# Kernel optimization log

Hardware: AMD Instinct MI355X
Metric: run time of the kernel (lower is better)

The kernel has to match this reference:

```python
import jax, jax.numpy as jnp
import numpy as np

N = 100000   # nodes
E = 1600000  # edges
G = 64       # graphs in batch
F_IN = 128
H = 128
SV = 64
AD = 32


def setup_inputs() -> dict:
    key = jax.random.key(0)
    ks = jax.random.split(key, 12)
    s = 0.05
    return {
        "x": jax.random.normal(ks[0], (N, F_IN), jnp.float32),
        "edge_index": jax.random.randint(ks[1], (2, E), 0, N, dtype=jnp.int64),
        "batch": jnp.sort(jax.random.randint(ks[2], (N,), 0, G, dtype=jnp.int64)),
        "state_vector": jax.random.normal(ks[3], (G, SV), jnp.float32),
        "action": jax.random.normal(ks[4], (G, AD), jnp.float32),
        "W1": jax.random.normal(ks[5], (F_IN, H), jnp.float32) * s,
        "b1": jnp.zeros((H,), jnp.float32),
        "W2": jax.random.normal(ks[6], (H, H), jnp.float32) * s,
        "b2": jnp.zeros((H,), jnp.float32),
        "Wf1": jax.random.normal(ks[7], (H + SV + AD, 256), jnp.float32) * s,
        "bf1": jnp.zeros((256,), jnp.float32),
        "Wf2": jax.random.normal(ks[8], (256, 256), jnp.float32) * s,
        "bf2": jnp.zeros((256,), jnp.float32),
        "Wo": jax.random.normal(ks[9], (256, 1), jnp.float32) * s,
        "bo": jnp.zeros((1,), jnp.float32),
    }


def gcn_conv(x, W, b, src, dst, deg_inv_sqrt):
    # PyG GCNConv: h = x @ W; aggregate D^-1/2 (A+I) D^-1/2 h; + b
    h = x @ W
    norm = deg_inv_sqrt[src] * deg_inv_sqrt[dst]          # [E]
    agg = jax.ops.segment_sum(h[src] * norm[:, None], dst, num_segments=N)
    agg = agg + h * (deg_inv_sqrt * deg_inv_sqrt)[:, None]  # self loops
    return agg + b


def reference(x, edge_index, batch, state_vector, action,
              W1, b1, W2, b2, Wf1, bf1, Wf2, bf2, Wo, bo):
    src, dst = edge_index[0], edge_index[1]
    # degree after adding self loops (aggregation index = dst, PyG default flow)
    deg = jax.ops.segment_sum(jnp.ones((E,), jnp.float32), dst, num_segments=N) + 1.0
    deg_inv_sqrt = jax.lax.rsqrt(deg)

    h = jax.nn.relu(gcn_conv(x, W1, b1, src, dst, deg_inv_sqrt))
    h = jax.nn.relu(gcn_conv(h, W2, b2, src, dst, deg_inv_sqrt))

    # global_mean_pool over graph ids
    sums = jax.ops.segment_sum(h, batch, num_segments=G)
    cnts = jax.ops.segment_sum(jnp.ones((N,), jnp.float32), batch, num_segments=G)
    pooled = sums / jnp.maximum(cnts, 1.0)[:, None]       # [G, H]

    z = jnp.concatenate([pooled, state_vector, action], axis=1)  # [G, H+SV+AD]
    z = jax.nn.relu(z @ Wf1 + bf1)
    z = jax.nn.relu(z @ Wf2 + bf2)
    return z @ Wo + bo                                     # [G, 1]
```

## Files before the change

### kernel.cpp

```cpp
#include <hip/hip_runtime.h>
#include <hip/hip_bf16.h>
#include <stdint.h>

#define N_NODES 100000
#define N_EDGES 1600000
#define N_GRAPHS 64
#define HDIM 128

#define BUCKET_SHIFT 9
#define NBUCK ((N_NODES + 511) >> 9)
#define CAP 9216
#define SCAT_CHUNK 4096
#define SCAT_NBLK ((N_EDGES + SCAT_CHUNK - 1) / SCAT_CHUNK)

typedef __bf16 bf16x8 __attribute__((ext_vector_type(8)));
typedef float f32x4 __attribute__((ext_vector_type(4)));
typedef float f32x2 __attribute__((ext_vector_type(2)));

__global__ void init_kernel(int* __restrict__ gcur, float* __restrict__ psum) {
    int i = blockIdx.x * blockDim.x + threadIdx.x;
    if (i < NBUCK) gcur[i] = i * CAP;
    int j = i - NBUCK;
    if (j >= 0 && j < N_GRAPHS * HDIM) psum[j] = 0.f;
}

__global__ __launch_bounds__(256) void transpose_w2_kernel(const float* __restrict__ W1,
                                                           const float* __restrict__ W2,
                                                           __hip_bfloat16* __restrict__ Wt1,
                                                           __hip_bfloat16* __restrict__ Wt2) {
    int bid = blockIdx.x;
    const float* W = (bid < 64) ? W1 : W2;
    __hip_bfloat16* Wt = (bid < 64) ? Wt1 : Wt2;
    int bb = bid & 63;
    int n = bb * 2 + (threadIdx.x >> 7);
    int k = threadIdx.x & 127;
    Wt[n * 128 + k] = __float2bfloat16(W[k * 128 + n]);
}

__global__ __launch_bounds__(256) void scatter_kernel(const int* __restrict__ src,
                                                      const int* __restrict__ dst,
                                                      int* __restrict__ gcur,
                                                      int* __restrict__ sorted, int E) {
    __shared__ int hist[NBUCK];
    __shared__ int base_s[NBUCK];
    int tid = threadIdx.x;
    int e0 = blockIdx.x * SCAT_CHUNK;
    int sv[SCAT_CHUNK / 256], dv[SCAT_CHUNK / 256];
#pragma unroll
    for (int j = 0; j < SCAT_CHUNK / 256; j++) {
        int e = e0 + (j << 8) + tid;
        if (e < E) { sv[j] = src[e]; dv[j] = dst[e]; } else { sv[j] = -1; dv[j] = -1; }
    }
    if (tid < NBUCK) hist[tid] = 0;
    __syncthreads();
#pragma unroll
    for (int j = 0; j < SCAT_CHUNK / 256; j++)
        if (dv[j] >= 0) atomicAdd(&hist[dv[j] >> BUCKET_SHIFT], 1);
    __syncthreads();
    if (tid < NBUCK) {
        int c = hist[tid];
        base_s[tid] = (c > 0) ? atomicAdd(&gcur[tid], c) : 0;
    }
    __syncthreads();
    if (tid < NBUCK) hist[tid] = 0;
    __syncthreads();
#pragma unroll
    for (int j = 0; j < SCAT_CHUNK / 256; j++) {
        if (dv[j] >= 0) {
            int b = dv[j] >> BUCKET_SHIFT;
            int idx = atomicAdd(&hist[b], 1);
            sorted[base_s[b] + idx] = ((dv[j] & 511) << 17) | sv[j];
        }
    }
}

__global__ __launch_bounds__(256) void bucket_build_kernel(const int* __restrict__ sorted,
                                                           const int* __restrict__ gcur,
                                                           int2* __restrict__ rs2,
                                                           float* __restrict__ dis,
                                                           int* __restrict__ csr_src) {
    __shared__ int cnt[512];
    __shared__ int excl[512];
    __shared__ int ps[256];
    int b = blockIdx.x, tid = threadIdx.x;
    cnt[tid] = 0; cnt[tid + 256] = 0;
    __syncthreads();
    int node0 = b << BUCKET_SHIFT;
    int lo = b * CAP, hi = gcur[b];
    for (int i = lo + tid; i < hi; i += 256)
        atomicAdd(&cnt[((unsigned)sorted[i]) >> 17], 1);
    __syncthreads();
    int c0 = cnt[2 * tid], c1 = cnt[2 * tid + 1];
    ps[tid] = c0 + c1;
    __syncthreads();
#pragma unroll
    for (int off = 1; off < 256; off <<= 1) {
        int t = (tid >= off) ? ps[tid - off] : 0;
        __syncthreads();
        ps[tid] += t;
        __syncthreads();
    }
    int pex = ps[tid] - (c0 + c1);
    excl[2 * tid] = pex;
    excl[2 * tid + 1] = pex + c0;
    __syncthreads();
#pragma unroll
    for (int k = 0; k < 2; k++) {
        int li = tid + k * 256;
        int node = node0 + li;
        if (node < N_NODES) {
            int st = lo + excl[li];
            int c = cnt[li];
            rs2[node] = make_int2(st, st + c);
            dis[node] = rsqrtf((float)c + 1.0f);
        }
    }
    cnt[tid] = 0; cnt[tid + 256] = 0;
    __syncthreads();
    for (int i = lo + tid; i < hi; i += 256) {
        int v = sorted[i];
        int li = ((unsigned)v) >> 17;
        int idx = atomicAdd(&cnt[li], 1);
        csr_src[lo + excl[li] + idx] = v & 0x1FFFF;
    }
}

__global__ void graph_bounds_kernel(const int* __restrict__ batch, int* __restrict__ gstart,
                                    int n, int G) {
    int i = blockIdx.x * blockDim.x + threadIdx.x;
    if (i >= n) return;
    int b = batch[i];
    int prev = (i == 0) ? -1 : batch[i - 1];
    for (int g = prev + 1; g <= b; ++g) gstart[g] = i;
    if (i == n - 1) {
        for (int g = b + 1; g <= G; ++g) gstart[g] = n;
    }
}

template<bool A_FP32>
__global__ __launch_bounds__(256) void gemm_mfma_kernel(const void* __restrict__ Av,
                                                        const __hip_bfloat16* __restrict__ Wt,
                                                        const float* __restrict__ scale,
                                                        unsigned char* __restrict__ C, int nrows) {
    __shared__ float Cs[64 * 132];
    int tid = threadIdx.x;
    int wave = tid >> 6, lane = tid & 63;
    int quad = lane >> 4, l16 = lane & 15;
    int row0 = blockIdx.x * 64;
    int arow = row0 + wave * 16 + l16;
    int arow_c = min(arow, nrows - 1);

    const __hip_bfloat16* A16 = (const __hip_bfloat16*)Av;
    const float* A32 = (const float*)Av;

    f32x4 acc[8];
#pragma unroll
    for (int t = 0; t < 8; t++) acc[t] = (f32x4){0.f, 0.f, 0.f, 0.f};

#pragma unroll
    for (int kt = 0; kt < 4; kt++) {
        int kbase = kt * 32 + quad * 8;
        union { bf16x8 v; __hip_bfloat16 h[8]; uint4 u; } au;
        if (A_FP32) {
            const float* ap = A32 + (size_t)arow_c * 128 + kbase;
            float4 u0 = *(const float4*)ap;
            float4 u1 = *(const float4*)(ap + 4);
            au.h[0] = __float2bfloat16(u0.x); au.h[1] = __float2bfloat16(u0.y);
            au.h[2] = __float2bfloat16(u0.z); au.h[3] = __float2bfloat16(u0.w);
            au.h[4] = __float2bfloat16(u1.x); au.h[5] = __float2bfloat16(u1.y);
            au.h[6] = __float2bfloat16(u1.z); au.h[7] = __float2bfloat16(u1.w);
        } else {
            au.u = *(const uint4*)(A16 + (size_t)arow_c * 128 + kbase);
        }
#pragma unroll
        for (int t = 0; t < 8; t++) {
            bf16x8 b = *(const bf16x8*)(Wt + (size_t)(t * 16 + l16) * 128 + kbase);
            acc[t] = __builtin_amdgcn_mfma_f32_16x16x32_bf16(au.v, b, acc[t], 0, 0, 0);
        }
    }

    int rbase = wave * 16 + quad * 4;
    float s[4];
#pragma unroll
    for (int r = 0; r < 4; r++) s[r] = scale[min(row0 + rbase + r, nrows - 1)];
#pragma unroll
    for (int t = 0; t < 8; t++) {
#pragma unroll
        for (int r = 0; r < 4; r++)
            Cs[(rbase + r) * 132 + t * 16 + l16] = acc[t][r] * s[r];
    }
    __syncthreads();

#pragma unroll
    for (int p = 0; p < 4; p++) {
        int g = p * 256 + tid;
        int row = g >> 4, c8 = (g & 15) * 8;
        int grow = row0 + row;
        if (grow < nrows) {
            const float* cp = &Cs[row * 132 + c8];
            float4 v0 = *(const float4*)cp;
            float4 v1 = *(const float4*)(cp + 4);
            int w0 = __builtin_amdgcn_cvt_pk_fp8_f32(v0.x, v0.y, 0, false);
            w0 = __builtin_amdgcn_cvt_pk_fp8_f32(v0.z, v0.w, w0, true);
            int w1 = __builtin_amdgcn_cvt_pk_fp8_f32(v1.x, v1.y, 0, false);
            w1 = __builtin_amdgcn_cvt_pk_fp8_f32(v1.z, v1.w, w1, true);
            *(uint2*)(C + (size_t)grow * 128 + c8) = make_uint2((unsigned)w0, (unsigned)w1);
        }
    }
}

__device__ __forceinline__ void accum8(float* acc, uint2 u) {
    f32x2 d0 = __builtin_amdgcn_cvt_pk_f32_fp8((int)u.x, false);
    f32x2 d1 = __builtin_amdgcn_cvt_pk_f32_fp8((int)u.x, true);
    f32x2 d2 = __builtin_amdgcn_cvt_pk_f32_fp8((int)u.y, false);
    f32x2 d3 = __builtin_amdgcn_cvt_pk_f32_fp8((int)u.y, true);
    acc[0] += d0[0]; acc[1] += d0[1]; acc[2] += d1[0]; acc[3] += d1[1];
    acc[4] += d2[0]; acc[5] += d2[1]; acc[6] += d3[0]; acc[7] += d3[1];
}

__global__ __launch_bounds__(256) void agg_kernel(const unsigned char* __restrict__ h8,
                                                  const float* __restrict__ dis,
                                                  const int2* __restrict__ rs2,
                                                  const int* __restrict__ csr_src,
                                                  const float* __restrict__ bias,
                                                  __hip_bfloat16* __restrict__ out, int n) {
    int node = blockIdx.x * 4 + (threadIdx.x >> 6);
    if (node >= n) return;
    int lane = threadIdx.x & 63;
    int q = lane >> 4, f = lane & 15;
    float acc[8];
#pragma unroll
    for (int j = 0; j < 8; j++) acc[j] = 0.f;
    int2 se = rs2[node];
    int i = se.x, i1 = se.y;
    for (; i + 8 <= i1; i += 8) {
        int s0 = csr_src[i + q];
        int s1 = csr_src[i + 4 + q];
        uint2 u0 = *(const uint2*)(h8 + (size_t)s0 * 128 + f * 8);
        uint2 u1 = *(const uint2*)(h8 + (size_t)s1 * 128 + f * 8);
        accum8(acc, u0);
        accum8(acc, u1);
    }
    for (; i + 4 <= i1; i += 4) {
        int s = csr_src[i + q];
        uint2 u = *(const uint2*)(h8 + (size_t)s * 128 + f * 8);
        accum8(acc, u);
    }
    if (i < i1) {
        bool valid = (i + q) < i1;
        int e = valid ? (i + q) : (i1 - 1);
        int s = csr_src[e];
        uint2 u = *(const uint2*)(h8 + (size_t)s * 128 + f * 8);
        if (valid) accum8(acc, u);
    }
    if (q == 0) {
        uint2 u = *(const uint2*)(h8 + (size_t)node * 128 + f * 8);
        accum8(acc, u);
    }
#pragma unroll
    for (int j = 0; j < 8; j++) {
        float v = acc[j];
        v += __shfl_down(v, 32, 64);
        v += __shfl_down(v, 16, 64);
        acc[j] = v;
    }
    if (q == 0) {
        float dn = dis[node];
        float4 b0 = *(const float4*)(bias + f * 8);
        float4 b1 = *(const float4*)(bias + f * 8 + 4);
        float r0 = fmaxf(fmaf(acc[0], dn, b0.x), 0.f);
        float r1 = fmaxf(fmaf(acc[1], dn, b0.y), 0.f);
        float r2 = fmaxf(fmaf(acc[2], dn, b0.z), 0.f);
        float r3 = fmaxf(fmaf(acc[3], dn, b0.w), 0.f);
        float r4 = fmaxf(fmaf(acc[4], dn, b1.x), 0.f);
        float r5 = fmaxf(fmaf(acc[5], dn, b1.y), 0.f);
        float r6 = fmaxf(fmaf(acc[6], dn, b1.z), 0.f);
        float r7 = fmaxf(fmaf(acc[7], dn, b1.w), 0.f);
        __hip_bfloat162 p0 = __float22bfloat162_rn(make_float2(r0, r1));
        __hip_bfloat162 p1 = __float22bfloat162_rn(make_float2(r2, r3));
        __hip_bfloat162 p2 = __float22bfloat162_rn(make_float2(r4, r5));
        __hip_bfloat162 p3 = __float22bfloat162_rn(make_float2(r6, r7));
        uint4 pk;
        pk.x = *(unsigned int*)&p0; pk.y = *(unsigned int*)&p1;
        pk.z = *(unsigned int*)&p2; pk.w = *(unsigned int*)&p3;
        *(uint4*)(out + (size_t)node * 128 + f * 8) = pk;
    }
}

#define POOL_ROWS 128
__global__ __launch_bounds__(256) void pool_kernel(const __hip_bfloat16* __restrict__ h,
                                                   const int* __restrict__ batch,
                                                   const int* __restrict__ gstart,
                                                   float* __restrict__ psum, int n) {
    __shared__ float red[16 * 128];
    int tid = threadIdx.x;
    int rr = tid >> 4, fg = tid & 15;
    int r0 = blockIdx.x * POOL_ROWS;
    if (r0 >= n) return;
    int r1 = min(n, r0 + POOL_ROWS);
    int g = batch[r0];
    int seg_lo = r0;
    while (seg_lo < r1) {
        while (gstart[g + 1] <= seg_lo) g++;
        int seg_hi = min(r1, gstart[g + 1]);
        float a[8];
#pragma unroll
        for (int j = 0; j < 8; j++) a[j] = 0.f;
        for (int r = seg_lo + rr; r < seg_hi; r += 16) {
            uint4 u = *(const uint4*)(h + (size_t)r * 128 + fg * 8);
            float2 f0 = __bfloat1622float2(*(__hip_bfloat162*)&u.x);
            float2 f1 = __bfloat1622float2(*(__hip_bfloat162*)&u.y);
            float2 f2 = __bfloat1622float2(*(__hip_bfloat162*)&u.z);
            float2 f3 = __bfloat1622float2(*(__hip_bfloat162*)&u.w);
            a[0] += f0.x; a[1] += f0.y; a[2] += f1.x; a[3] += f1.y;
            a[4] += f2.x; a[5] += f2.y; a[6] += f3.x; a[7] += f3.y;
        }
        *(float4*)&red[rr * 128 + fg * 8] = make_float4(a[0], a[1], a[2], a[3]);
        *(float4*)&red[rr * 128 + fg * 8 + 4] = make_float4(a[4], a[5], a[6], a[7]);
        __syncthreads();
        if (tid < 128) {
            float s = 0.f;
#pragma unroll
            for (int k = 0; k < 16; k++) s += red[k * 128 + tid];
            atomicAdd(&psum[g * 128 + tid], s);
        }
        __syncthreads();
        seg_lo = seg_hi;
    }
}

__global__ __launch_bounds__(256) void mlp_kernel(const float* __restrict__ psum,
                                                  const int* __restrict__ gstart,
                                                  const float* __restrict__ sv,
                                                  const float* __restrict__ act,
                                                  const float* __restrict__ Wf1,
                                                  const float* __restrict__ bf1,
                                                  const float* __restrict__ Wf2,
                                                  const float* __restrict__ bf2,
                                                  const float* __restrict__ Wo,
                                                  const float* __restrict__ bo,
                                                  float* __restrict__ out) {
    int g = blockIdx.x, tid = threadIdx.x;
    __shared__ float z[224];
    __shared__ float z1[256];
    __shared__ float red[256];
    if (tid < 128) {
        int c = gstart[g + 1] - gstart[g];
        float cnt = fmaxf((float)c, 1.f);
        z[tid] = psum[g * 128 + tid] / cnt;
    } else if (tid < 192) {
        z[tid] = sv[g * 64 + (tid - 128)];
    } else if (tid < 224) {
        z[tid] = act[g * 32 + (tid - 192)];
    }
    __syncthreads();
    float a = bf1[tid];
    for (int k = 0; k < 224; k++) a = fmaf(z[k], Wf1[k * 256 + tid], a);
    z1[tid] = fmaxf(a, 0.f);
    __syncthreads();
    float b = bf2[tid];
    for (int k = 0; k < 256; k++) b = fmaf(z1[k], Wf2[k * 256 + tid], b);
    b = fmaxf(b, 0.f);
    red[tid] = b * Wo[tid];
    __syncthreads();
    for (int off = 128; off > 0; off >>= 1) {
        if (tid < off) red[tid] += red[tid + off];
        __syncthreads();
    }
    if (tid == 0) out[g] = red[0] + bo[0];
}

extern "C" void kernel_launch(void* const* d_in, const int* in_sizes, int n_in,
                              void* d_out, int out_size, void* d_ws, size_t ws_size,
                              hipStream_t stream) {
    const float* x   = (const float*)d_in[0];
    const int*   eidx = (const int*)d_in[1];
    const int*   batch = (const int*)d_in[2];
    const float* sv  = (const float*)d_in[3];
    const float* act = (const float*)d_in[4];
    const float* W1  = (const float*)d_in[5];
    const float* b1  = (const float*)d_in[6];
    const float* W2  = (const float*)d_in[7];
    const float* b2  = (const float*)d_in[8];
    const float* Wf1 = (const float*)d_in[9];
    const float* bf1 = (const float*)d_in[10];
    const float* Wf2 = (const float*)d_in[11];
    const float* bf2 = (const float*)d_in[12];
    const float* Wo  = (const float*)d_in[13];
    const float* bo  = (const float*)d_in[14];
    float* out = (float*)d_out;

    const int* srcp = eidx;
    const int* dstp = eidx + N_EDGES;

    char* w = (char*)d_ws;
    int* gcur = (int*)w;               w += (size_t)NBUCK * 4;
    float* psum = (float*)w;           w += (size_t)N_GRAPHS * HDIM * 4;
    int2* rs2 = (int2*)w;              w += (size_t)N_NODES * 8;
    float* dis = (float*)w;            w += (size_t)N_NODES * 4;
    int* gstart = (int*)w;             w += (size_t)(N_GRAPHS + 1) * 4;
    w = (char*)(((uintptr_t)w + 255) & ~(uintptr_t)255);
    int* csr_src = (int*)w;            w += (size_t)NBUCK * CAP * 4;
    w = (char*)(((uintptr_t)w + 255) & ~(uintptr_t)255);
    int* sorted = (int*)w;             w += (size_t)NBUCK * CAP * 4;
    w = (char*)(((uintptr_t)w + 255) & ~(uintptr_t)255);
    __hip_bfloat16* Wt1 = (__hip_bfloat16*)w;   w += (size_t)HDIM * HDIM * 2;
    __hip_bfloat16* Wt2 = (__hip_bfloat16*)w;   w += (size_t)HDIM * HDIM * 2;
    w = (char*)(((uintptr_t)w + 255) & ~(uintptr_t)255);
    unsigned char* hbuf = (unsigned char*)w;    w += (size_t)N_NODES * HDIM;
    w = (char*)(((uintptr_t)w + 255) & ~(uintptr_t)255);
    __hip_bfloat16* abuf = (__hip_bfloat16*)w;  w += (size_t)N_NODES * HDIM * 2;

    init_kernel<<<(NBUCK + N_GRAPHS * HDIM + 255) / 256, 256, 0, stream>>>(gcur, psum);
    transpose_w2_kernel<<<128, 256, 0, stream>>>(W1, W2, Wt1, Wt2);

    scatter_kernel<<<SCAT_NBLK, 256, 0, stream>>>(srcp, dstp, gcur, sorted, N_EDGES);
    bucket_build_kernel<<<NBUCK, 256, 0, stream>>>(sorted, gcur, rs2, dis, csr_src);
    graph_bounds_kernel<<<(N_NODES + 255) / 256, 256, 0, stream>>>(batch, gstart, N_NODES, N_GRAPHS);

    int gemm_blocks = (N_NODES + 63) / 64;
    int agg_blocks = (N_NODES + 3) / 4;

    gemm_mfma_kernel<true><<<gemm_blocks, 256, 0, stream>>>(x, Wt1, dis, hbuf, N_NODES);
    agg_kernel<<<agg_blocks, 256, 0, stream>>>(hbuf, dis, rs2, csr_src, b1, abuf, N_NODES);
    gemm_mfma_kernel<false><<<gemm_blocks, 256, 0, stream>>>(abuf, Wt2, dis, hbuf, N_NODES);
    agg_kernel<<<agg_blocks, 256, 0, stream>>>(hbuf, dis, rs2, csr_src, b2, abuf, N_NODES);

    pool_kernel<<<(N_NODES + POOL_ROWS - 1) / POOL_ROWS, 256, 0, stream>>>(abuf, batch, gstart, psum, N_NODES);
    mlp_kernel<<<N_GRAPHS, 256, 0, stream>>>(psum, gstart, sv, act, Wf1, bf1, Wf2, bf2, Wo, bo, out);
}
```

Before: 347.4 us.

## Merge setup kernels, stage bucket edges in LDS, double scatter chunk

Folds init, weight transpose and graph-bounds computation into one setup kernel, which removes two launches. The bucket-build kernel now copies each bucket's edges into shared memory once instead of reading global memory twice. The scatter chunk size is doubled, which halves the block count and per-block histogram overhead but raises register pressure and lowers parallelism. The extra 36KB of LDS per block may reduce occupancy of bucket_build.

```diff
diff --git a/kernel.cpp b/kernel.cpp
--- a/kernel.cpp
+++ b/kernel.cpp
@@ -10,32 +10,48 @@
 #define BUCKET_SHIFT 9
 #define NBUCK ((N_NODES + 511) >> 9)
 #define CAP 9216
-#define SCAT_CHUNK 4096
+#define SCAT_CHUNK 8192
 #define SCAT_NBLK ((N_EDGES + SCAT_CHUNK - 1) / SCAT_CHUNK)
+#define GB_NBLK ((N_NODES + 255) / 256)
 
 typedef __bf16 bf16x8 __attribute__((ext_vector_type(8)));
 typedef float f32x4 __attribute__((ext_vector_type(4)));
 typedef float f32x2 __attribute__((ext_vector_type(2)));
 
-__global__ void init_kernel(int* __restrict__ gcur, float* __restrict__ psum) {
-    int i = blockIdx.x * blockDim.x + threadIdx.x;
-    if (i < NBUCK) gcur[i] = i * CAP;
-    int j = i - NBUCK;
-    if (j >= 0 && j < N_GRAPHS * HDIM) psum[j] = 0.f;
-}
-
-__global__ __launch_bounds__(256) void transpose_w2_kernel(const float* __restrict__ W1,
-                                                           const float* __restrict__ W2,
-                                                           __hip_bfloat16* __restrict__ Wt1,
-                                                           __hip_bfloat16* __restrict__ Wt2) {
+__global__ __launch_bounds__(256) void setup_kernel(const int* __restrict__ batch,
+                                                    int* __restrict__ gstart,
+                                                    const float* __restrict__ W1,
+                                                    const float* __restrict__ W2,
+                                                    __hip_bfloat16* __restrict__ Wt1,
+                                                    __hip_bfloat16* __restrict__ Wt2,
+                                                    int* __restrict__ gcur,
+                                                    float* __restrict__ psum) {
     int bid = blockIdx.x;
-    const float* W = (bid < 64) ? W1 : W2;
-    __hip_bfloat16* Wt = (bid < 64) ? Wt1 : Wt2;
-    int bb = bid & 63;
-    int n = bb * 2 + (threadIdx.x >> 7);
-    int k = threadIdx.x & 127;
-    Wt[n * 128 + k] = __float2bfloat16(W[k * 128 + n]);
-}
+    if (bid < GB_NBLK) {
+        int i = bid * 256 + threadIdx.x;
+        if (i >= N_NODES) return;
+        int b = batch[i];
+        int prev = (i == 0) ? -1 : batch[i - 1];
+        for (int g = prev + 1; g <= b; ++g) gstart[g] = i;
+        if (i == N_NODES - 1) {
+            for (int g = b + 1; g <= N_GRAPHS; ++g) gstart[g] = N_NODES;
+        }
+    } else if (bid < GB_NBLK + 128) {
+        int t = bid - GB_NBLK;
+        const float* W = (t < 64) ? W1 : W2;
+        __hip_bfloat16* Wt = (t < 64) ? Wt1 : Wt2;
+        int bb = t & 63;
+        int n = bb * 2 + (threadIdx.x >> 7);
+        int k = threadIdx.x & 127;
+        Wt[n * 128 + k] = __float2bfloat16(W[k * 128 + n]);
+    } else {
+        int i = (bid - GB_NBLK - 128) * 256 + threadIdx.x;
+        if (i < NBUCK) gcur[i] = i * CAP;
+        int j = i - NBUCK;
+        if (j >= 0 && j < N_GRAPHS * HDIM) psum[j] = 0.f;
+    }
+}
+#define SETUP_NBLK (GB_NBLK + 128 + (NBUCK + N_GRAPHS * HDIM + 255) / 256)
 
 __global__ __launch_bounds__(256) void scatter_kernel(const int* __restrict__ src,
                                                       const int* __restrict__ dst,
@@ -79,16 +95,19 @@
                                                            int2* __restrict__ rs2,
                                                            float* __restrict__ dis,
                                                            int* __restrict__ csr_src) {
+    __shared__ int edges[CAP];
     __shared__ int cnt[512];
     __shared__ int excl[512];
     __shared__ int ps[256];
     int b = blockIdx.x, tid = threadIdx.x;
     cnt[tid] = 0; cnt[tid + 256] = 0;
-    __syncthreads();
     int node0 = b << BUCKET_SHIFT;
     int lo = b * CAP, hi = gcur[b];
-    for (int i = lo + tid; i < hi; i += 256)
-        atomicAdd(&cnt[((unsigned)sorted[i]) >> 17], 1);
+    int ne = hi - lo;
+    for (int i = tid; i < ne; i += 256) edges[i] = sorted[lo + i];
+    __syncthreads();
+    for (int i = tid; i < ne; i += 256)
+        atomicAdd(&cnt[((unsigned)edges[i]) >> 17], 1);
     __syncthreads();
     int c0 = cnt[2 * tid], c1 = cnt[2 * tid + 1];
     ps[tid] = c0 + c1;
@@ -117,23 +136,11 @@
     }
     cnt[tid] = 0; cnt[tid + 256] = 0;
     __syncthreads();
-    for (int i = lo + tid; i < hi; i += 256) {
-        int v = sorted[i];
+    for (int i = tid; i < ne; i += 256) {
+        int v = edges[i];
         int li = ((unsigned)v) >> 17;
         int idx = atomicAdd(&cnt[li], 1);
         csr_src[lo + excl[li] + idx] = v & 0x1FFFF;
-    }
-}
-
-__global__ void graph_bounds_kernel(const int* __restrict__ batch, int* __restrict__ gstart,
-                                    int n, int G) {
-    int i = blockIdx.x * blockDim.x + threadIdx.x;
-    if (i >= n) return;
-    int b = batch[i];
-    int prev = (i == 0) ? -1 : batch[i - 1];
-    for (int g = prev + 1; g <= b; ++g) gstart[g] = i;
-    if (i == n - 1) {
-        for (int g = b + 1; g <= G; ++g) gstart[g] = n;
     }
 }
 
@@ -411,12 +418,10 @@
     w = (char*)(((uintptr_t)w + 255) & ~(uintptr_t)255);
     __hip_bfloat16* abuf = (__hip_bfloat16*)w;  w += (size_t)N_NODES * HDIM * 2;
 
-    init_kernel<<<(NBUCK + N_GRAPHS * HDIM + 255) / 256, 256, 0, stream>>>(gcur, psum);
-    transpose_w2_kernel<<<128, 256, 0, stream>>>(W1, W2, Wt1, Wt2);
+    setup_kernel<<<SETUP_NBLK, 256, 0, stream>>>(batch, gstart, W1, W2, Wt1, Wt2, gcur, psum);
 
     scatter_kernel<<<SCAT_NBLK, 256, 0, stream>>>(srcp, dstp, gcur, sorted, N_EDGES);
     bucket_build_kernel<<<NBUCK, 256, 0, stream>>>(sorted, gcur, rs2, dis, csr_src);
-    graph_bounds_kernel<<<(N_NODES + 255) / 256, 256, 0, stream>>>(batch, gstart, N_NODES, N_GRAPHS);
 
     int gemm_blocks = (N_NODES + 63) / 64;
     int agg_blocks = (N_NODES + 3) / 4;
```

After: 331.5 us. 1.05x faster.
